# Kernel optimization log

Measured on AMD Instinct MI355X. Metric: run time of the kernel, lower is better.

Reference implementation:

```python
import jax, jax.numpy as jnp
import numpy as np

N_POINTS = 300000
NUM_CLUSTERS = 64
LATENT_DIM = 32
DET = 1e-16  # matches `det` in update_gamma


def setup_inputs() -> dict:
    key = jax.random.key(0)
    k1, k2, k3 = jax.random.split(key, 3)
    mu_phi = jax.random.normal(k1, (N_POINTS, LATENT_DIM), dtype=jnp.float32)
    # per-node scalar log-variance (encoder's gcn_logstddev has output dim 1)
    log_cov_phi = jax.random.normal(k2, (N_POINTS, 1), dtype=jnp.float32) * 0.1
    pi_k = jnp.ones((NUM_CLUSTERS,), jnp.float32) / NUM_CLUSTERS
    mu_k = jax.random.normal(k3, (NUM_CLUSTERS, LATENT_DIM), dtype=jnp.float32)
    log_cov_k = jnp.full((NUM_CLUSTERS, 1), 0.1, jnp.float32)
    return {"mu_phi": mu_phi, "log_cov_phi": log_cov_phi, "pi_k": pi_k,
            "mu_k": mu_k, "log_cov_k": log_cov_k, "P": LATENT_DIM}


def _sq_dist(a, b):
    # ||a_i - b_k||^2 via expansion; avoids materializing [N,K,P]
    return (jnp.sum(a * a, axis=1)[:, None]
            - 2.0 * (a @ b.T)
            + jnp.sum(b * b, axis=1)[None, :])


def reference(mu_phi, log_cov_phi, pi_k, mu_k, log_cov_k, P):
    Pf = jnp.float32(P)
    lcp = log_cov_phi[:, 0]          # [N]
    lck = log_cov_k[:, 0]            # [K]
    # --- update_gamma: KL[i,k] between q(z_i) and cluster k (isotropic) ---
    sq = _sq_dist(mu_phi, mu_k)      # [N,K]
    inv_cov_k = jnp.exp(-lck)[None, :]
    KL = 0.5 * (Pf * (lck[None, :] - lcp[:, None]) - Pf
                + Pf * jnp.exp(lcp)[:, None] * inv_cov_k
                + sq * inv_cov_k)    # [N,K]
    w = pi_k[None, :] * jnp.exp(-KL)
    gamma = w / jnp.sum(w, axis=1, keepdims=True) + DET  # [N,K]
    # --- update_others: M-step using the new gamma ---
    N_k = jnp.sum(gamma, axis=0)                          # [K]
    pi_new = N_k / jnp.float32(gamma.shape[0])
    mu_new = (gamma.T @ mu_phi) / N_k[:, None]            # [K,P]
    sq2 = _sq_dist(mu_phi, mu_new)                        # [N,K]
    diff = Pf * jnp.exp(lcp)[:, None] + sq2               # [N,K]
    cov_new = jnp.sum(gamma * diff, axis=0) / (Pf * N_k)  # [K]
    log_cov_new = jnp.log(cov_new)[:, None]               # [K,1]
    return gamma, pi_new, mu_new, log_cov_new
```

## Files before the change

### kernel.cpp

```cpp
#include <hip/hip_runtime.h>
#include <math.h>

#define NPTS 300000
#define K 64
#define P 32
#define DETC 1e-16f
#define WS_FLOATS (K + K + K * P)
#define NCOPIES 32

#define NBLOCKS 2048
#define NTHREADS 256
#define NWAVES (NBLOCKS * (NTHREADS / 64))
#define CHUNK ((NPTS + NWAVES - 1) / NWAVES)

#define DPP_ADD(v, ctrl)                                                     \
    v += __int_as_float(__builtin_amdgcn_update_dpp(                         \
        0, __float_as_int(v), (ctrl), 0xF, 0xF, true))

__device__ __forceinline__ float rl(float x, int lane) {
    return __int_as_float(__builtin_amdgcn_readlane(__float_as_int(x), lane));
}

__global__ __launch_bounds__(NTHREADS, 4) void em_pass(
    const float* __restrict__ mu_phi,
    const float* __restrict__ log_cov_phi,
    const float* __restrict__ pi_k,
    const float* __restrict__ mu_k,
    const float* __restrict__ log_cov_k,
    float* __restrict__ gamma_out,
    float* __restrict__ out_tail,
    float* __restrict__ ws)
{
    const int lane = threadIdx.x & 63;
    const int wave = threadIdx.x >> 6;
    const int gw = __builtin_amdgcn_readfirstlane(blockIdx.x * (NTHREADS / 64) + wave);

    const float lck  = log_cov_k[lane];
    const float icov = __expf(-lck);
    const float pik  = pi_k[lane];

    float mk2[P];
    float n2k = 0.f;
#pragma unroll
    for (int d = 0; d < P; ++d) {
        const float m = mu_k[lane * P + d];
        mk2[d] = icov * m;
        n2k = fmaf(m, m, n2k);
    }
    const float Ak     = 0.5f * (32.f * lck - 32.f + icov * n2k) - __logf(pik);
    const float negAk  = -Ak;
    const float nhicov = -0.5f * icov;

    float accN = 0.f, accS = 0.f;
    float accM[P];
#pragma unroll
    for (int d = 0; d < P; ++d) accM[d] = 0.f;

    const int start = gw * CHUNK;
    const int end0  = (start + CHUNK < NPTS) ? (start + CHUNK) : NPTS;
    const int cnt   = end0 - start;

    if (cnt > 0) {
        float u_v = 0.f, bl_v = 0.f;
        if (lane < cnt) {
            const float4* r4 =
                reinterpret_cast<const float4*>(mu_phi + (size_t)(start + lane) * P);
            float n2 = 0.f;
#pragma unroll 1
            for (int q = 0; q < 8; q += 4) {
                float4 a = r4[q], b = r4[q + 1], c = r4[q + 2], e = r4[q + 3];
                n2 = fmaf(a.x, a.x, n2); n2 = fmaf(a.y, a.y, n2);
                n2 = fmaf(a.z, a.z, n2); n2 = fmaf(a.w, a.w, n2);
                n2 = fmaf(b.x, b.x, n2); n2 = fmaf(b.y, b.y, n2);
                n2 = fmaf(b.z, b.z, n2); n2 = fmaf(b.w, b.w, n2);
                n2 = fmaf(c.x, c.x, n2); n2 = fmaf(c.y, c.y, n2);
                n2 = fmaf(c.z, c.z, n2); n2 = fmaf(c.w, c.w, n2);
                n2 = fmaf(e.x, e.x, n2); n2 = fmaf(e.y, e.y, n2);
                n2 = fmaf(e.z, e.z, n2); n2 = fmaf(e.w, e.w, n2);
            }
            const float lcp = log_cov_phi[start + lane];
            u_v  = fmaf(32.f, __expf(lcp), n2);
            bl_v = 16.f * lcp;
        }

#pragma unroll 2
        for (int p = 0; p < cnt; ++p) {
            const int i = start + p;
            const float u_s  = rl(u_v, p);
            const float bl_s = rl(bl_v, p);
            const float* row = mu_phi + (size_t)i * P;

            float d0 = 0.f, d1 = 0.f, d2 = 0.f, d3 = 0.f;
#pragma unroll
            for (int d = 0; d < P; d += 4) {
                d0 = fmaf(row[d + 0], mk2[d + 0], d0);
                d1 = fmaf(row[d + 1], mk2[d + 1], d1);
                d2 = fmaf(row[d + 2], mk2[d + 2], d2);
                d3 = fmaf(row[d + 3], mk2[d + 3], d3);
            }
            const float dot = (d0 + d1) + (d2 + d3);

            const float tpart = fmaf(nhicov, u_s, negAk);
            const float w = __expf((dot + tpart) + bl_s);

            float v = w;
            DPP_ADD(v, 0xB1);
            DPP_ADD(v, 0x4E);
            DPP_ADD(v, 0x128);
            DPP_ADD(v, 0x124);
            const float sum = (rl(v, 0) + rl(v, 16)) + (rl(v, 32) + rl(v, 48));

            const float g = fmaf(w, __builtin_amdgcn_rcpf(sum), DETC);
            __builtin_nontemporal_store(g, gamma_out + (size_t)i * K + lane);

            accN += g;
            accS  = fmaf(g, u_s, accS);
#pragma unroll
            for (int d = 0; d < P; ++d) accM[d] = fmaf(g, row[d], accM[d]);
        }
    }

    __shared__ float red[WS_FLOATS];
    for (int idx = threadIdx.x; idx < WS_FLOATS; idx += NTHREADS) red[idx] = 0.f;
    __syncthreads();

    atomicAdd(&red[lane], accN);
    atomicAdd(&red[K + lane], accS);
#pragma unroll
    for (int d = 0; d < P; ++d) atomicAdd(&red[2 * K + d * K + lane], accM[d]);
    __syncthreads();

    float* wsc = ws + (size_t)(blockIdx.x & (NCOPIES - 1)) * WS_FLOATS;
    for (int idx = threadIdx.x; idx < WS_FLOATS; idx += NTHREADS)
        atomicAdd(&wsc[idx], red[idx]);
    __syncthreads();

    __shared__ int lastf;
    if (threadIdx.x == 0) {
        __threadfence();
        const int c = atomicAdd((int*)(ws + (size_t)NCOPIES * WS_FLOATS), 1);
        lastf = (c == NBLOCKS - 1);
    }
    __syncthreads();
    if (lastf) {
        __threadfence();
        for (int idx = threadIdx.x; idx < WS_FLOATS; idx += NTHREADS) {
            float s = 0.f;
#pragma unroll 4
            for (int c = 0; c < NCOPIES; ++c)
                s += __hip_atomic_load(&ws[(size_t)c * WS_FLOATS + idx],
                                       __ATOMIC_RELAXED, __HIP_MEMORY_SCOPE_AGENT);
            red[idx] = s;
        }
        __syncthreads();

        const int k = threadIdx.x;
        if (k < K) {
            const float Nk = red[k];
            const float S  = red[K + k];
            float* pi_new      = out_tail;
            float* mu_new      = out_tail + K;
            float* log_cov_new = out_tail + K + K * P;

            pi_new[k] = Nk / (float)NPTS;
            const float invN = 1.f / Nk;
            float m2 = 0.f;
#pragma unroll
            for (int d = 0; d < P; ++d) {
                const float md = red[2 * K + d * K + k] * invN;
                mu_new[k * P + d] = md;
                m2 = fmaf(md, md, m2);
            }
            const float cov = (S - Nk * m2) / (32.f * Nk);
            log_cov_new[k] = logf(cov);
        }
    }
}

extern "C" void kernel_launch(void* const* d_in, const int* in_sizes, int n_in,
                              void* d_out, int out_size, void* d_ws, size_t ws_size,
                              hipStream_t stream)
{
    const float* mu_phi      = (const float*)d_in[0];
    const float* log_cov_phi = (const float*)d_in[1];
    const float* pi_k        = (const float*)d_in[2];
    const float* mu_k        = (const float*)d_in[3];
    const float* log_cov_k   = (const float*)d_in[4];
    float* out = (float*)d_out;
    float* ws  = (float*)d_ws;

    hipMemsetAsync(ws, 0, ((size_t)NCOPIES * WS_FLOATS + 1) * sizeof(float), stream);
    em_pass<<<NBLOCKS, NTHREADS, 0, stream>>>(mu_phi, log_cov_phi, pi_k, mu_k,
                                              log_cov_k, out,
                                              out + (size_t)NPTS * K, ws);
}
```

Measured before the change: 245.7 us.

## Load each point row once per lane and broadcast via readlane

Each wave now takes a fixed 64-point tile. Every lane loads one full row of mu_phi into registers with vector loads, and the per-point loop broadcasts the row elements with readlane instead of having all lanes reload the row from memory (scalar/uniform loads) each iteration. The grid grows to about 4688 tiles/4 waves per block instead of 2048 fixed blocks with ~37-point chunks. This removes redundant per-iteration memory loads at the cost of 32 readlane instructions per point and more blocks, which means more global atomic reductions into the workspace.

```diff
diff --git a/kernel.cpp b/kernel.cpp
--- a/kernel.cpp
+++ b/kernel.cpp
@@ -8,10 +8,11 @@
 #define WS_FLOATS (K + K + K * P)
 #define NCOPIES 32
 
-#define NBLOCKS 2048
 #define NTHREADS 256
-#define NWAVES (NBLOCKS * (NTHREADS / 64))
-#define CHUNK ((NPTS + NWAVES - 1) / NWAVES)
+#define WPB (NTHREADS / 64)
+#define TILE 64
+#define NTILES ((NPTS + TILE - 1) / TILE)
+#define NBLOCKS ((NTILES + WPB - 1) / WPB)
 
 #define DPP_ADD(v, ctrl)                                                     \
     v += __int_as_float(__builtin_amdgcn_update_dpp(                         \
@@ -33,7 +34,7 @@
 {
     const int lane = threadIdx.x & 63;
     const int wave = threadIdx.x >> 6;
-    const int gw = __builtin_amdgcn_readfirstlane(blockIdx.x * (NTHREADS / 64) + wave);
+    const int gw = __builtin_amdgcn_readfirstlane(blockIdx.x * WPB + wave);
 
     const float lck  = log_cov_k[lane];
     const float icov = __expf(-lck);
@@ -56,68 +57,89 @@
 #pragma unroll
     for (int d = 0; d < P; ++d) accM[d] = 0.f;
 
-    const int start = gw * CHUNK;
-    const int end0  = (start + CHUNK < NPTS) ? (start + CHUNK) : NPTS;
-    const int cnt   = end0 - start;
-
-    if (cnt > 0) {
-        float u_v = 0.f, bl_v = 0.f;
-        if (lane < cnt) {
-            const float4* r4 =
-                reinterpret_cast<const float4*>(mu_phi + (size_t)(start + lane) * P);
-            float n2 = 0.f;
-#pragma unroll 1
-            for (int q = 0; q < 8; q += 4) {
-                float4 a = r4[q], b = r4[q + 1], c = r4[q + 2], e = r4[q + 3];
-                n2 = fmaf(a.x, a.x, n2); n2 = fmaf(a.y, a.y, n2);
-                n2 = fmaf(a.z, a.z, n2); n2 = fmaf(a.w, a.w, n2);
-                n2 = fmaf(b.x, b.x, n2); n2 = fmaf(b.y, b.y, n2);
-                n2 = fmaf(b.z, b.z, n2); n2 = fmaf(b.w, b.w, n2);
-                n2 = fmaf(c.x, c.x, n2); n2 = fmaf(c.y, c.y, n2);
-                n2 = fmaf(c.z, c.z, n2); n2 = fmaf(c.w, c.w, n2);
-                n2 = fmaf(e.x, e.x, n2); n2 = fmaf(e.y, e.y, n2);
-                n2 = fmaf(e.z, e.z, n2); n2 = fmaf(e.w, e.w, n2);
-            }
-            const float lcp = log_cov_phi[start + lane];
-            u_v  = fmaf(32.f, __expf(lcp), n2);
-            bl_v = 16.f * lcp;
-        }
+    const int start = gw * TILE;
+    const int cnt   = (NPTS - start < TILE) ? (NPTS - start) : TILE;
+
+    const int ridx = start + ((lane < cnt) ? lane : 0);
+    const float4* r4p = reinterpret_cast<const float4*>(mu_phi + (size_t)ridx * P);
+    float4 c0 = r4p[0], c1 = r4p[1], c2 = r4p[2], c3 = r4p[3];
+    float4 c4 = r4p[4], c5 = r4p[5], c6 = r4p[6], c7 = r4p[7];
+
+    float n2 = 0.f;
+#define N2ACC(q) n2 = fmaf(q.x,q.x,n2); n2 = fmaf(q.y,q.y,n2); \
+                 n2 = fmaf(q.z,q.z,n2); n2 = fmaf(q.w,q.w,n2)
+    N2ACC(c0); N2ACC(c1); N2ACC(c2); N2ACC(c3);
+    N2ACC(c4); N2ACC(c5); N2ACC(c6); N2ACC(c7);
+#undef N2ACC
+    const float lcp  = log_cov_phi[ridx];
+    const float u_v  = fmaf(32.f, __expf(lcp), n2);
+    const float bl_v = 16.f * lcp;
 
 #pragma unroll 2
-        for (int p = 0; p < cnt; ++p) {
-            const int i = start + p;
-            const float u_s  = rl(u_v, p);
-            const float bl_s = rl(bl_v, p);
-            const float* row = mu_phi + (size_t)i * P;
-
-            float d0 = 0.f, d1 = 0.f, d2 = 0.f, d3 = 0.f;
-#pragma unroll
-            for (int d = 0; d < P; d += 4) {
-                d0 = fmaf(row[d + 0], mk2[d + 0], d0);
-                d1 = fmaf(row[d + 1], mk2[d + 1], d1);
-                d2 = fmaf(row[d + 2], mk2[d + 2], d2);
-                d3 = fmaf(row[d + 3], mk2[d + 3], d3);
-            }
-            const float dot = (d0 + d1) + (d2 + d3);
-
-            const float tpart = fmaf(nhicov, u_s, negAk);
-            const float w = __expf((dot + tpart) + bl_s);
-
-            float v = w;
-            DPP_ADD(v, 0xB1);
-            DPP_ADD(v, 0x4E);
-            DPP_ADD(v, 0x128);
-            DPP_ADD(v, 0x124);
-            const float sum = (rl(v, 0) + rl(v, 16)) + (rl(v, 32) + rl(v, 48));
-
-            const float g = fmaf(w, __builtin_amdgcn_rcpf(sum), DETC);
-            __builtin_nontemporal_store(g, gamma_out + (size_t)i * K + lane);
-
-            accN += g;
-            accS  = fmaf(g, u_s, accS);
-#pragma unroll
-            for (int d = 0; d < P; ++d) accM[d] = fmaf(g, row[d], accM[d]);
-        }
+    for (int p = 0; p < cnt; ++p) {
+        const int i = start + p;
+        const float u_s  = rl(u_v, p);
+        const float bl_s = rl(bl_v, p);
+
+        const float s00 = rl(c0.x, p), s01 = rl(c0.y, p), s02 = rl(c0.z, p), s03 = rl(c0.w, p);
+        const float s04 = rl(c1.x, p), s05 = rl(c1.y, p), s06 = rl(c1.z, p), s07 = rl(c1.w, p);
+        const float s08 = rl(c2.x, p), s09 = rl(c2.y, p), s10 = rl(c2.z, p), s11 = rl(c2.w, p);
+        const float s12 = rl(c3.x, p), s13 = rl(c3.y, p), s14 = rl(c3.z, p), s15 = rl(c3.w, p);
+        const float s16 = rl(c4.x, p), s17 = rl(c4.y, p), s18 = rl(c4.z, p), s19 = rl(c4.w, p);
+        const float s20 = rl(c5.x, p), s21 = rl(c5.y, p), s22 = rl(c5.z, p), s23 = rl(c5.w, p);
+        const float s24 = rl(c6.x, p), s25 = rl(c6.y, p), s26 = rl(c6.z, p), s27 = rl(c6.w, p);
+        const float s28 = rl(c7.x, p), s29 = rl(c7.y, p), s30 = rl(c7.z, p), s31 = rl(c7.w, p);
+
+        float d0 = 0.f, d1 = 0.f, d2 = 0.f, d3 = 0.f;
+        d0 = fmaf(s00, mk2[0],  d0); d1 = fmaf(s01, mk2[1],  d1);
+        d2 = fmaf(s02, mk2[2],  d2); d3 = fmaf(s03, mk2[3],  d3);
+        d0 = fmaf(s04, mk2[4],  d0); d1 = fmaf(s05, mk2[5],  d1);
+        d2 = fmaf(s06, mk2[6],  d2); d3 = fmaf(s07, mk2[7],  d3);
+        d0 = fmaf(s08, mk2[8],  d0); d1 = fmaf(s09, mk2[9],  d1);
+        d2 = fmaf(s10, mk2[10], d2); d3 = fmaf(s11, mk2[11], d3);
+        d0 = fmaf(s12, mk2[12], d0); d1 = fmaf(s13, mk2[13], d1);
+        d2 = fmaf(s14, mk2[14], d2); d3 = fmaf(s15, mk2[15], d3);
+        d0 = fmaf(s16, mk2[16], d0); d1 = fmaf(s17, mk2[17], d1);
+        d2 = fmaf(s18, mk2[18], d2); d3 = fmaf(s19, mk2[19], d3);
+        d0 = fmaf(s20, mk2[20], d0); d1 = fmaf(s21, mk2[21], d1);
+        d2 = fmaf(s22, mk2[22], d2); d3 = fmaf(s23, mk2[23], d3);
+        d0 = fmaf(s24, mk2[24], d0); d1 = fmaf(s25, mk2[25], d1);
+        d2 = fmaf(s26, mk2[26], d2); d3 = fmaf(s27, mk2[27], d3);
+        d0 = fmaf(s28, mk2[28], d0); d1 = fmaf(s29, mk2[29], d1);
+        d2 = fmaf(s30, mk2[30], d2); d3 = fmaf(s31, mk2[31], d3);
+        const float dot = (d0 + d1) + (d2 + d3);
+
+        const float tpart = fmaf(nhicov, u_s, negAk);
+        const float w = __expf((dot + tpart) + bl_s);
+
+        float v = w;
+        DPP_ADD(v, 0xB1);
+        DPP_ADD(v, 0x4E);
+        DPP_ADD(v, 0x128);
+        DPP_ADD(v, 0x124);
+        const float sum = (rl(v, 0) + rl(v, 16)) + (rl(v, 32) + rl(v, 48));
+
+        const float g = fmaf(w, __builtin_amdgcn_rcpf(sum), DETC);
+        __builtin_nontemporal_store(g, gamma_out + (size_t)i * K + lane);
+
+        accN += g;
+        accS  = fmaf(g, u_s, accS);
+        accM[0]  = fmaf(g, s00, accM[0]);  accM[1]  = fmaf(g, s01, accM[1]);
+        accM[2]  = fmaf(g, s02, accM[2]);  accM[3]  = fmaf(g, s03, accM[3]);
+        accM[4]  = fmaf(g, s04, accM[4]);  accM[5]  = fmaf(g, s05, accM[5]);
+        accM[6]  = fmaf(g, s06, accM[6]);  accM[7]  = fmaf(g, s07, accM[7]);
+        accM[8]  = fmaf(g, s08, accM[8]);  accM[9]  = fmaf(g, s09, accM[9]);
+        accM[10] = fmaf(g, s10, accM[10]); accM[11] = fmaf(g, s11, accM[11]);
+        accM[12] = fmaf(g, s12, accM[12]); accM[13] = fmaf(g, s13, accM[13]);
+        accM[14] = fmaf(g, s14, accM[14]); accM[15] = fmaf(g, s15, accM[15]);
+        accM[16] = fmaf(g, s16, accM[16]); accM[17] = fmaf(g, s17, accM[17]);
+        accM[18] = fmaf(g, s18, accM[18]); accM[19] = fmaf(g, s19, accM[19]);
+        accM[20] = fmaf(g, s20, accM[20]); accM[21] = fmaf(g, s21, accM[21]);
+        accM[22] = fmaf(g, s22, accM[22]); accM[23] = fmaf(g, s23, accM[23]);
+        accM[24] = fmaf(g, s24, accM[24]); accM[25] = fmaf(g, s25, accM[25]);
+        accM[26] = fmaf(g, s26, accM[26]); accM[27] = fmaf(g, s27, accM[27]);
+        accM[28] = fmaf(g, s28, accM[28]); accM[29] = fmaf(g, s29, accM[29]);
+        accM[30] = fmaf(g, s30, accM[30]); accM[31] = fmaf(g, s31, accM[31]);
     }
 
     __shared__ float red[WS_FLOATS];
```

Result: faster. 227.2 us (-7.5%).

## Compute E-step distances and M-step sums with split-bf16 MFMA tiles

Applied to the files above, without the earlier changes.

Replaces the per-point scalar FMA dot products and per-dimension accumulation with MFMA matrix instructions on 16-row tiles. Inputs are split into hi/lo bf16 pairs and three MFMAs per product approximate fp32 accuracy. The work split changes to one 64-point tile per wave, which raises the block count, and launch bounds drop to 2 blocks per CU. The aim is to cut VALU work in both the distance and the gamma^T·mu reduction, at the cost of extra packing, shuffles, many more blocks doing workspace atomics, and a small loss of precision.

```diff
diff --git a/kernel.cpp b/kernel.cpp
--- a/kernel.cpp
+++ b/kernel.cpp
@@ -8,20 +8,43 @@
 #define WS_FLOATS (K + K + K * P)
 #define NCOPIES 32
 
-#define NBLOCKS 2048
 #define NTHREADS 256
-#define NWAVES (NBLOCKS * (NTHREADS / 64))
-#define CHUNK ((NPTS + NWAVES - 1) / NWAVES)
+#define WPB (NTHREADS / 64)
+#define TILE 64
+#define NTILES ((NPTS + TILE - 1) / TILE)
+#define NBLOCKS ((NTILES + WPB - 1) / WPB)
+
+typedef __attribute__((ext_vector_type(8)))  short    bf16x8;
+typedef __attribute__((ext_vector_type(4)))  float    f32x4;
+typedef __attribute__((ext_vector_type(16))) float    f32x16;
+typedef __attribute__((ext_vector_type(4)))  unsigned u32x4;
+
+#define MF16(a, b, c) __builtin_amdgcn_mfma_f32_16x16x32_bf16(a, b, c, 0, 0, 0)
+#define MF32(a, b, c) __builtin_amdgcn_mfma_f32_32x32x16_bf16(a, b, c, 0, 0, 0)
 
 #define DPP_ADD(v, ctrl)                                                     \
     v += __int_as_float(__builtin_amdgcn_update_dpp(                         \
         0, __float_as_int(v), (ctrl), 0xF, 0xF, true))
-
-__device__ __forceinline__ float rl(float x, int lane) {
-    return __int_as_float(__builtin_amdgcn_readlane(__float_as_int(x), lane));
+#define DPP16(v) do { DPP_ADD(v, 0xB1); DPP_ADD(v, 0x4E);                    \
+                      DPP_ADD(v, 0x128); DPP_ADD(v, 0x124); } while (0)
+
+__device__ __forceinline__ unsigned pkbf(float a, float b) {
+    unsigned ua = __float_as_uint(a), ub = __float_as_uint(b);
+    ua = (ua + 0x7fffu + ((ua >> 16) & 1u)) >> 16;
+    ub = (ub + 0x7fffu + ((ub >> 16) & 1u)) & 0xffff0000u;
+    return ua | ub;
 }
-
-__global__ __launch_bounds__(NTHREADS, 4) void em_pass(
+#define PKHL(xa, xb, dh, dl) do {                                            \
+    dh = pkbf((xa), (xb));                                                   \
+    dl = pkbf((xa) - __uint_as_float(dh << 16),                              \
+              (xb) - __uint_as_float(dh & 0xffff0000u)); } while (0)
+
+__device__ __forceinline__ bf16x8 mkfrag(unsigned a, unsigned b, unsigned c, unsigned d) {
+    u32x4 t = {a, b, c, d};
+    return __builtin_bit_cast(bf16x8, t);
+}
+
+__global__ __launch_bounds__(NTHREADS, 2) void em_pass(
     const float* __restrict__ mu_phi,
     const float* __restrict__ log_cov_phi,
     const float* __restrict__ pi_k,
@@ -33,90 +56,197 @@
 {
     const int lane = threadIdx.x & 63;
     const int wave = threadIdx.x >> 6;
-    const int gw = __builtin_amdgcn_readfirstlane(blockIdx.x * (NTHREADS / 64) + wave);
-
-    const float lck  = log_cov_k[lane];
-    const float icov = __expf(-lck);
-    const float pik  = pi_k[lane];
-
-    float mk2[P];
-    float n2k = 0.f;
-#pragma unroll
-    for (int d = 0; d < P; ++d) {
-        const float m = mu_k[lane * P + d];
-        mk2[d] = icov * m;
-        n2k = fmaf(m, m, n2k);
-    }
-    const float Ak     = 0.5f * (32.f * lck - 32.f + icov * n2k) - __logf(pik);
-    const float negAk  = -Ak;
-    const float nhicov = -0.5f * icov;
-
-    float accN = 0.f, accS = 0.f;
-    float accM[P];
-#pragma unroll
-    for (int d = 0; d < P; ++d) accM[d] = 0.f;
-
-    const int start = gw * CHUNK;
-    const int end0  = (start + CHUNK < NPTS) ? (start + CHUNK) : NPTS;
-    const int cnt   = end0 - start;
-
-    if (cnt > 0) {
-        float u_v = 0.f, bl_v = 0.f;
-        if (lane < cnt) {
-            const float4* r4 =
-                reinterpret_cast<const float4*>(mu_phi + (size_t)(start + lane) * P);
-            float n2 = 0.f;
-#pragma unroll 1
-            for (int q = 0; q < 8; q += 4) {
-                float4 a = r4[q], b = r4[q + 1], c = r4[q + 2], e = r4[q + 3];
-                n2 = fmaf(a.x, a.x, n2); n2 = fmaf(a.y, a.y, n2);
-                n2 = fmaf(a.z, a.z, n2); n2 = fmaf(a.w, a.w, n2);
-                n2 = fmaf(b.x, b.x, n2); n2 = fmaf(b.y, b.y, n2);
-                n2 = fmaf(b.z, b.z, n2); n2 = fmaf(b.w, b.w, n2);
-                n2 = fmaf(c.x, c.x, n2); n2 = fmaf(c.y, c.y, n2);
-                n2 = fmaf(c.z, c.z, n2); n2 = fmaf(c.w, c.w, n2);
-                n2 = fmaf(e.x, e.x, n2); n2 = fmaf(e.y, e.y, n2);
-                n2 = fmaf(e.z, e.z, n2); n2 = fmaf(e.w, e.w, n2);
-            }
-            const float lcp = log_cov_phi[start + lane];
-            u_v  = fmaf(32.f, __expf(lcp), n2);
-            bl_v = 16.f * lcp;
+    const int gw = __builtin_amdgcn_readfirstlane(blockIdx.x * WPB + wave);
+
+    const int l15 = lane & 15;
+    const int g4  = lane >> 4;
+    const int l31 = lane & 31;
+    const int h   = lane >> 5;
+    const int b4  = g4 & 1;
+
+    float nh0, nh1, nh2, nh3;
+    float Ak0, Ak1, Ak2, Ak3;
+    bf16x8 Bh0, Bh1, Bh2, Bh3, Bl0, Bl1, Bl2, Bl3;
+#define MKB(kt, BH, BL, NHI, AKV) do {                                       \
+        const int ck = l15 + 16 * (kt);                                      \
+        const float4 m0 = *(const float4*)(mu_k + ck * P + 8 * g4);          \
+        const float4 m1 = *(const float4*)(mu_k + ck * P + 8 * g4 + 4);      \
+        float n2p = 0.f;                                                     \
+        n2p = fmaf(m0.x, m0.x, n2p); n2p = fmaf(m0.y, m0.y, n2p);            \
+        n2p = fmaf(m0.z, m0.z, n2p); n2p = fmaf(m0.w, m0.w, n2p);            \
+        n2p = fmaf(m1.x, m1.x, n2p); n2p = fmaf(m1.y, m1.y, n2p);            \
+        n2p = fmaf(m1.z, m1.z, n2p); n2p = fmaf(m1.w, m1.w, n2p);            \
+        n2p += __shfl_xor(n2p, 16);  n2p += __shfl_xor(n2p, 32);             \
+        const float lk = log_cov_k[ck];                                      \
+        const float ic = __expf(-lk);                                        \
+        NHI = -0.5f * ic;                                                    \
+        AKV = 0.5f * (32.f * lk - 32.f + ic * n2p) - __logf(pi_k[ck]);       \
+        unsigned q0, q1, q2, q3, r0, r1, r2, r3;                             \
+        PKHL(ic * m0.x, ic * m0.y, q0, r0);                                  \
+        PKHL(ic * m0.z, ic * m0.w, q1, r1);                                  \
+        PKHL(ic * m1.x, ic * m1.y, q2, r2);                                  \
+        PKHL(ic * m1.z, ic * m1.w, q3, r3);                                  \
+        BH = mkfrag(q0, q1, q2, q3); BL = mkfrag(r0, r1, r2, r3); } while (0)
+    MKB(0, Bh0, Bl0, nh0, Ak0);
+    MKB(1, Bh1, Bl1, nh1, Ak1);
+    MKB(2, Bh2, Bl2, nh2, Ak2);
+    MKB(3, Bh3, Bl3, nh3, Ak3);
+#undef MKB
+
+    float accN0 = 0.f, accN1 = 0.f, accN2 = 0.f, accN3 = 0.f;
+    float accS0 = 0.f, accS1 = 0.f, accS2 = 0.f, accS3 = 0.f;
+    f32x16 accM0 = {};
+    f32x16 accM1 = {};
+
+    const int start = gw * TILE;
+    const int cnt   = (NPTS - start < TILE) ? (NPTS - start) : TILE;
+    const int nPt   = cnt >> 4;
+
+    for (int pt = 0; pt < nPt; ++pt) {
+        const int rbase = start + pt * 16;
+
+        const float* prow = mu_phi + (size_t)(rbase + l15) * P + 8 * g4;
+        const float4 p0 = *(const float4*)(prow);
+        const float4 p1 = *(const float4*)(prow + 4);
+        const float* pcol = mu_phi + (size_t)(rbase + 8 * h) * P + l31;
+        const float t0 = pcol[0 * P], t1 = pcol[1 * P], t2 = pcol[2 * P], t3 = pcol[3 * P];
+        const float t4 = pcol[4 * P], t5 = pcol[5 * P], t6 = pcol[6 * P], t7 = pcol[7 * P];
+
+        float n2 = 0.f;
+        n2 = fmaf(p0.x, p0.x, n2); n2 = fmaf(p0.y, p0.y, n2);
+        n2 = fmaf(p0.z, p0.z, n2); n2 = fmaf(p0.w, p0.w, n2);
+        n2 = fmaf(p1.x, p1.x, n2); n2 = fmaf(p1.y, p1.y, n2);
+        n2 = fmaf(p1.z, p1.z, n2); n2 = fmaf(p1.w, p1.w, n2);
+        n2 += __shfl_xor(n2, 16); n2 += __shfl_xor(n2, 32);
+        const float lcpv = log_cov_phi[rbase + l15];
+        const float u_l  = fmaf(32.f, __expf(lcpv), n2);
+        const float bl_l = 16.f * lcpv;
+
+        unsigned a0, a1, a2, a3, e0, e1, e2, e3;
+        PKHL(p0.x, p0.y, a0, e0); PKHL(p0.z, p0.w, a1, e1);
+        PKHL(p1.x, p1.y, a2, e2); PKHL(p1.z, p1.w, a3, e3);
+        const bf16x8 Ah = mkfrag(a0, a1, a2, a3), Al = mkfrag(e0, e1, e2, e3);
+
+        f32x4 s0 = {0.f, 0.f, 0.f, 0.f}, s1 = {0.f, 0.f, 0.f, 0.f};
+        f32x4 s2 = {0.f, 0.f, 0.f, 0.f}, s3 = {0.f, 0.f, 0.f, 0.f};
+        s0 = MF16(Ah, Bh0, s0); s0 = MF16(Ah, Bl0, s0); s0 = MF16(Al, Bh0, s0);
+        s1 = MF16(Ah, Bh1, s1); s1 = MF16(Ah, Bl1, s1); s1 = MF16(Al, Bh1, s1);
+        s2 = MF16(Ah, Bh2, s2); s2 = MF16(Ah, Bl2, s2); s2 = MF16(Al, Bh2, s2);
+        s3 = MF16(Ah, Bh3, s3); s3 = MF16(Ah, Bl3, s3); s3 = MF16(Al, Bh3, s3);
+
+        const int sl = 4 * g4;
+        const float u0 = __shfl(u_l, sl),     u1 = __shfl(u_l, sl + 1);
+        const float u2 = __shfl(u_l, sl + 2), u3 = __shfl(u_l, sl + 3);
+        const float b0 = __shfl(bl_l, sl),     b1 = __shfl(bl_l, sl + 1);
+        const float b2 = __shfl(bl_l, sl + 2), b3 = __shfl(bl_l, sl + 3);
+
+        const float w00 = __expf(s0[0] + fmaf(nh0, u0, b0 - Ak0));
+        const float w01 = __expf(s0[1] + fmaf(nh0, u1, b1 - Ak0));
+        const float w02 = __expf(s0[2] + fmaf(nh0, u2, b2 - Ak0));
+        const float w03 = __expf(s0[3] + fmaf(nh0, u3, b3 - Ak0));
+        const float w10 = __expf(s1[0] + fmaf(nh1, u0, b0 - Ak1));
+        const float w11 = __expf(s1[1] + fmaf(nh1, u1, b1 - Ak1));
+        const float w12 = __expf(s1[2] + fmaf(nh1, u2, b2 - Ak1));
+        const float w13 = __expf(s1[3] + fmaf(nh1, u3, b3 - Ak1));
+        const float w20 = __expf(s2[0] + fmaf(nh2, u0, b0 - Ak2));
+        const float w21 = __expf(s2[1] + fmaf(nh2, u1, b1 - Ak2));
+        const float w22 = __expf(s2[2] + fmaf(nh2, u2, b2 - Ak2));
+        const float w23 = __expf(s2[3] + fmaf(nh2, u3, b3 - Ak2));
+        const float w30 = __expf(s3[0] + fmaf(nh3, u0, b0 - Ak3));
+        const float w31 = __expf(s3[1] + fmaf(nh3, u1, b1 - Ak3));
+        const float w32 = __expf(s3[2] + fmaf(nh3, u2, b2 - Ak3));
+        const float w33 = __expf(s3[3] + fmaf(nh3, u3, b3 - Ak3));
+
+        float r0 = (w00 + w10) + (w20 + w30);
+        float r1 = (w01 + w11) + (w21 + w31);
+        float r2 = (w02 + w12) + (w22 + w32);
+        float r3 = (w03 + w13) + (w23 + w33);
+        DPP16(r0); DPP16(r1); DPP16(r2); DPP16(r3);
+        const float q0 = __builtin_amdgcn_rcpf(r0);
+        const float q1 = __builtin_amdgcn_rcpf(r1);
+        const float q2 = __builtin_amdgcn_rcpf(r2);
+        const float q3 = __builtin_amdgcn_rcpf(r3);
+
+        const float g00 = fmaf(w00, q0, DETC), g01 = fmaf(w01, q1, DETC);
+        const float g02 = fmaf(w02, q2, DETC), g03 = fmaf(w03, q3, DETC);
+        const float g10 = fmaf(w10, q0, DETC), g11 = fmaf(w11, q1, DETC);
+        const float g12 = fmaf(w12, q2, DETC), g13 = fmaf(w13, q3, DETC);
+        const float g20 = fmaf(w20, q0, DETC), g21 = fmaf(w21, q1, DETC);
+        const float g22 = fmaf(w22, q2, DETC), g23 = fmaf(w23, q3, DETC);
+        const float g30 = fmaf(w30, q0, DETC), g31 = fmaf(w31, q1, DETC);
+        const float g32 = fmaf(w32, q2, DETC), g33 = fmaf(w33, q3, DETC);
+
+        float* gp = gamma_out + (size_t)(rbase + sl) * K + l15;
+        __builtin_nontemporal_store(g00, gp + 0 * K +  0);
+        __builtin_nontemporal_store(g10, gp + 0 * K + 16);
+        __builtin_nontemporal_store(g20, gp + 0 * K + 32);
+        __builtin_nontemporal_store(g30, gp + 0 * K + 48);
+        __builtin_nontemporal_store(g01, gp + 1 * K +  0);
+        __builtin_nontemporal_store(g11, gp + 1 * K + 16);
+        __builtin_nontemporal_store(g21, gp + 1 * K + 32);
+        __builtin_nontemporal_store(g31, gp + 1 * K + 48);
+        __builtin_nontemporal_store(g02, gp + 2 * K +  0);
+        __builtin_nontemporal_store(g12, gp + 2 * K + 16);
+        __builtin_nontemporal_store(g22, gp + 2 * K + 32);
+        __builtin_nontemporal_store(g32, gp + 2 * K + 48);
+        __builtin_nontemporal_store(g03, gp + 3 * K +  0);
+        __builtin_nontemporal_store(g13, gp + 3 * K + 16);
+        __builtin_nontemporal_store(g23, gp + 3 * K + 32);
+        __builtin_nontemporal_store(g33, gp + 3 * K + 48);
+
+        accN0 += (g00 + g01) + (g02 + g03);
+        accN1 += (g10 + g11) + (g12 + g13);
+        accN2 += (g20 + g21) + (g22 + g23);
+        accN3 += (g30 + g31) + (g32 + g33);
+        accS0 = fmaf(g00, u0, accS0); accS0 = fmaf(g01, u1, accS0);
+        accS0 = fmaf(g02, u2, accS0); accS0 = fmaf(g03, u3, accS0);
+        accS1 = fmaf(g10, u0, accS1); accS1 = fmaf(g11, u1, accS1);
+        accS1 = fmaf(g12, u2, accS1); accS1 = fmaf(g13, u3, accS1);
+        accS2 = fmaf(g20, u0, accS2); accS2 = fmaf(g21, u1, accS2);
+        accS2 = fmaf(g22, u2, accS2); accS2 = fmaf(g23, u3, accS2);
+        accS3 = fmaf(g30, u0, accS3); accS3 = fmaf(g31, u1, accS3);
+        accS3 = fmaf(g32, u2, accS3); accS3 = fmaf(g33, u3, accS3);
+
+        unsigned f0, f1, f2, f3, x0, x1, x2, x3;
+        PKHL(t0, t1, f0, x0); PKHL(t2, t3, f1, x1);
+        PKHL(t4, t5, f2, x2); PKHL(t6, t7, f3, x3);
+        const bf16x8 Tp = mkfrag(f0, f1, f2, f3), Tl = mkfrag(x0, x1, x2, x3);
+
+        {
+            const float o0 = b4 ? g10 : g00, o1 = b4 ? g11 : g01;
+            const float o2 = b4 ? g12 : g02, o3 = b4 ? g13 : g03;
+            const float z0 = b4 ? g00 : g10, z1 = b4 ? g01 : g11;
+            const float z2 = b4 ? g02 : g12, z3 = b4 ? g03 : g13;
+            unsigned oh0, ol0, oh1, ol1, zh0, zl0, zh1, zl1;
+            PKHL(o0, o1, oh0, ol0); PKHL(o2, o3, oh1, ol1);
+            PKHL(z0, z1, zh0, zl0); PKHL(z2, z3, zh1, zl1);
+            const unsigned rh0 = __shfl_xor(zh0, 16), rh1 = __shfl_xor(zh1, 16);
+            const unsigned rl0 = __shfl_xor(zl0, 16), rl1 = __shfl_xor(zl1, 16);
+            const bf16x8 Bgh = mkfrag(b4 ? rh0 : oh0, b4 ? rh1 : oh1,
+                                      b4 ? oh0 : rh0, b4 ? oh1 : rh1);
+            const bf16x8 Bgl = mkfrag(b4 ? rl0 : ol0, b4 ? rl1 : ol1,
+                                      b4 ? ol0 : rl0, b4 ? ol1 : rl1);
+            accM0 = MF32(Tp, Bgh, accM0);
+            accM0 = MF32(Tp, Bgl, accM0);
+            accM0 = MF32(Tl, Bgh, accM0);
         }
-
-#pragma unroll 2
-        for (int p = 0; p < cnt; ++p) {
-            const int i = start + p;
-            const float u_s  = rl(u_v, p);
-            const float bl_s = rl(bl_v, p);
-            const float* row = mu_phi + (size_t)i * P;
-
-            float d0 = 0.f, d1 = 0.f, d2 = 0.f, d3 = 0.f;
-#pragma unroll
-            for (int d = 0; d < P; d += 4) {
-                d0 = fmaf(row[d + 0], mk2[d + 0], d0);
-                d1 = fmaf(row[d + 1], mk2[d + 1], d1);
-                d2 = fmaf(row[d + 2], mk2[d + 2], d2);
-                d3 = fmaf(row[d + 3], mk2[d + 3], d3);
-            }
-            const float dot = (d0 + d1) + (d2 + d3);
-
-            const float tpart = fmaf(nhicov, u_s, negAk);
-            const float w = __expf((dot + tpart) + bl_s);
-
-            float v = w;
-            DPP_ADD(v, 0xB1);
-            DPP_ADD(v, 0x4E);
-            DPP_ADD(v, 0x128);
-            DPP_ADD(v, 0x124);
-            const float sum = (rl(v, 0) + rl(v, 16)) + (rl(v, 32) + rl(v, 48));
-
-            const float g = fmaf(w, __builtin_amdgcn_rcpf(sum), DETC);
-            __builtin_nontemporal_store(g, gamma_out + (size_t)i * K + lane);
-
-            accN += g;
-            accS  = fmaf(g, u_s, accS);
-#pragma unroll
-            for (int d = 0; d < P; ++d) accM[d] = fmaf(g, row[d], accM[d]);
+        {
+            const float o0 = b4 ? g30 : g20, o1 = b4 ? g31 : g21;
+            const float o2 = b4 ? g32 : g22, o3 = b4 ? g33 : g23;
+            const float z0 = b4 ? g20 : g30, z1 = b4 ? g21 : g31;
+            const float z2 = b4 ? g22 : g32, z3 = b4 ? g23 : g33;
+            unsigned oh0, ol0, oh1, ol1, zh0, zl0, zh1, zl1;
+            PKHL(o0, o1, oh0, ol0); PKHL(o2, o3, oh1, ol1);
+            PKHL(z0, z1, zh0, zl0); PKHL(z2, z3, zh1, zl1);
+            const unsigned rh0 = __shfl_xor(zh0, 16), rh1 = __shfl_xor(zh1, 16);
+            const unsigned rl0 = __shfl_xor(zl0, 16), rl1 = __shfl_xor(zl1, 16);
+            const bf16x8 Bgh = mkfrag(b4 ? rh0 : oh0, b4 ? rh1 : oh1,
+                                      b4 ? oh0 : rh0, b4 ? oh1 : rh1);
+            const bf16x8 Bgl = mkfrag(b4 ? rl0 : ol0, b4 ? rl1 : ol1,
+                                      b4 ? ol0 : rl0, b4 ? ol1 : rl1);
+            accM1 = MF32(Tp, Bgh, accM1);
+            accM1 = MF32(Tp, Bgl, accM1);
+            accM1 = MF32(Tl, Bgh, accM1);
         }
     }
 
@@ -124,10 +254,16 @@
     for (int idx = threadIdx.x; idx < WS_FLOATS; idx += NTHREADS) red[idx] = 0.f;
     __syncthreads();
 
-    atomicAdd(&red[lane], accN);
-    atomicAdd(&red[K + lane], accS);
+    atomicAdd(&red[l15 +  0], accN0); atomicAdd(&red[l15 + 16], accN1);
+    atomicAdd(&red[l15 + 32], accN2); atomicAdd(&red[l15 + 48], accN3);
+    atomicAdd(&red[K + l15 +  0], accS0); atomicAdd(&red[K + l15 + 16], accS1);
+    atomicAdd(&red[K + l15 + 32], accS2); atomicAdd(&red[K + l15 + 48], accS3);
 #pragma unroll
-    for (int d = 0; d < P; ++d) atomicAdd(&red[2 * K + d * K + lane], accM[d]);
+    for (int r = 0; r < 16; ++r) {
+        const int d = (r & 3) + 8 * (r >> 2) + 4 * h;
+        atomicAdd(&red[2 * K + d * K + l31],      accM0[r]);
+        atomicAdd(&red[2 * K + d * K + l31 + 32], accM1[r]);
+    }
     __syncthreads();
 
     float* wsc = ws + (size_t)(blockIdx.x & (NCOPIES - 1)) * WS_FLOATS;
```

New measurement: 244.5 us. No clear change (-0.5%).
